# Performance work log

Hardware: AMD Instinct MI355X
Metric: run time of the kernel (lower is better)

Reference implementation:

```python
import jax, jax.numpy as jnp
import numpy as np
from jax.scipy.special import digamma, polygamma

N_ITERS = 100
TOL = 1e-3


def setup_inputs() -> dict:
    key = jax.random.key(0)
    x = jax.random.normal(key, (2_000_000, 10), dtype=jnp.float32)
    return {"x": x}


def reference(x):
    # x: [n, C] logits -> Dirichlet MLE over softmax probabilities
    p = jax.nn.softmax(x, axis=-1)            # [n, C]
    n = p.shape[0]
    m1 = p.mean(0)                            # [C] E[p]
    m2 = (p ** 2).mean(0)                     # [C] E[p^2]
    # method-of-moments initialization (as in the torch module)
    a0 = m1 * ((m1 - m2) / (m2 - m1 ** 2)).mean(-1)
    # loop-invariant sufficient statistic
    log_p_avg = jnp.log(p).mean(0)            # [C]

    def cond(carry):
        a, k, diff = carry
        return jnp.logical_and(k < N_ITERS, diff >= TOL)

    def body(carry):
        a, k, _ = carry
        g = (digamma(a.sum(-1)) - digamma(a) + log_p_avg) * n
        q = -n * polygamma(1, a)
        z = n * polygamma(1, a.sum(-1))
        q_inv = 1.0 / q
        b = (g * q_inv).sum(-1) / (1.0 / z + q_inv.sum(-1))
        a_new = a - (g - b) / q               # Newton step with rank-1 Hessian inverse
        diff = jnp.abs(a_new - a).sum()       # L1 norm, matches torch.norm(.,1)
        return (a_new, k + 1, diff)

    a, _, _ = jax.lax.while_loop(
        cond, body, (a0, jnp.int32(0), jnp.float32(jnp.inf))
    )
    return a.astype(jnp.float32)
```

## Files before the change

### kernel.cpp

```cpp
#include <hip/hip_runtime.h>
#include <math.h>

#define C 10
#define BLOCK 256
#define NBLOCKS 2048
#define TILE_ROWS 512
#define TILE_ELEMS (TILE_ROWS * C)
#define NSTATS (3 * C)


__device__ __forceinline__ void accum_row(const float* __restrict__ row,
                                          float* __restrict__ s1,
                                          float* __restrict__ s2,
                                          float* __restrict__ sl) {
  float v[C];
#pragma unroll
  for (int c = 0; c < C; c++) v[c] = row[c];
  float mx = v[0];
#pragma unroll
  for (int c = 1; c < C; c++) mx = fmaxf(mx, v[c]);
  float e[C], se = 0.f;
#pragma unroll
  for (int c = 0; c < C; c++) { v[c] -= mx; e[c] = __expf(v[c]); se += e[c]; }
  float inv = 1.0f / se;
  float lse = __logf(se);
#pragma unroll
  for (int c = 0; c < C; c++) {
    float p = e[c] * inv;
    s1[c] += p;
    s2[c] = fmaf(p, p, s2[c]);
    sl[c] += v[c] - lse;
  }
}

__global__ __launch_bounds__(BLOCK) void dir_stats_kernel(
    const float* __restrict__ x, float* __restrict__ partials,
    int nrows, int ntiles, int tailStart, int nblocks) {
  __shared__ float tile[TILE_ELEMS];
  const int tid = threadIdx.x;

  float s1[C], s2[C], sl[C];
#pragma unroll
  for (int c = 0; c < C; c++) { s1[c] = 0.f; s2[c] = 0.f; sl[c] = 0.f; }

  for (int t = blockIdx.x; t < ntiles; t += nblocks) {
    const float4* __restrict__ src = (const float4*)(x + (size_t)t * TILE_ELEMS);
    float4* dst = (float4*)tile;
#pragma unroll
    for (int i = 0; i < TILE_ELEMS / 4 / BLOCK; i++)
      dst[tid + i * BLOCK] = src[tid + i * BLOCK];
    __syncthreads();
#pragma unroll
    for (int r = 0; r < TILE_ROWS / BLOCK; r++)
      accum_row(tile + (size_t)(r * BLOCK + tid) * C, s1, s2, sl);
    __syncthreads();
  }

  if (blockIdx.x == nblocks - 1) {
    for (int rr = tailStart + tid; rr < nrows; rr += BLOCK)
      accum_row(x + (size_t)rr * C, s1, s2, sl);
  }

  const int lane = tid & 63;
  const int wave = tid >> 6;
  __shared__ float red[4][NSTATS];
#pragma unroll
  for (int c = 0; c < C; c++) {
    float v1 = s1[c], v2 = s2[c], v3 = sl[c];
#pragma unroll
    for (int off = 32; off >= 1; off >>= 1) {
      v1 += __shfl_down(v1, off);
      v2 += __shfl_down(v2, off);
      v3 += __shfl_down(v3, off);
    }
    if (lane == 0) {
      red[wave][c] = v1;
      red[wave][C + c] = v2;
      red[wave][2 * C + c] = v3;
    }
  }
  __syncthreads();
  if (tid < NSTATS) {
    float tot = red[0][tid] + red[1][tid] + red[2][tid] + red[3][tid];
    partials[(size_t)tid * nblocks + blockIdx.x] = tot;
  }
}


__device__ __forceinline__ void digtri8(double x, double& dg, double& tg) {
  double i0 = 1.0 / x,         i1 = 1.0 / (x + 1.0);
  double i2 = 1.0 / (x + 2.0), i3 = 1.0 / (x + 3.0);
  double i4 = 1.0 / (x + 4.0), i5 = 1.0 / (x + 5.0);
  double i6 = 1.0 / (x + 6.0), i7 = 1.0 / (x + 7.0);
  double rd = (i0 + i1) + (i2 + i3) + ((i4 + i5) + (i6 + i7));
  double rt = (i0 * i0 + i1 * i1) + (i2 * i2 + i3 * i3) +
              ((i4 * i4 + i5 * i5) + (i6 * i6 + i7 * i7));
  double y = x + 8.0;
  double yi = 1.0 / y, f = yi * yi;
  dg = log(y) - 0.5 * yi
     - f * (1.0 / 12 - f * (1.0 / 120 - f * (1.0 / 252 - f * (1.0 / 240 - f * (1.0 / 132)))))
     - rd;
  tg = rt + yi + 0.5 * f
     + f * yi * (1.0 / 6 - f * (1.0 / 30 - f * (1.0 / 42 - f * (1.0 / 30))));
}

__device__ __forceinline__ double wsum16(double v) {
#pragma unroll
  for (int off = 1; off < 16; off <<= 1) v += __shfl_xor(v, off);
  return v;
}

__global__ __launch_bounds__(1024) void dir_newton_kernel(
    const float* __restrict__ partials, float* __restrict__ out,
    int nparts, double nrows) {
  __shared__ double tot[NSTATS];
  const int tid = threadIdx.x;

  {
    const int j = tid >> 5;
    const int k = tid & 31;
    double s = 0.0;
    if (j < NSTATS) {
      const float* __restrict__ base = partials + (size_t)j * nparts;
#pragma unroll 8
      for (int b = k; b < nparts; b += 32)
        s += (double)base[b];
    }
#pragma unroll
    for (int off = 16; off >= 1; off >>= 1) s += __shfl_xor(s, off);
    if (j < NSTATS && k == 0) tot[j] = s;
  }
  __syncthreads();

  if (tid < 16) {
    const int c = tid;
    const bool act = (c < C);
    const double n = nrows;
    double m1 = 0.0, m2 = 0.0, lpa = 0.0;
    if (act) {
      m1 = tot[c] / n;
      m2 = tot[C + c] / n;
      lpa = tot[2 * C + c] / n;
    }
    double ratio = act ? (m1 - m2) / (m2 - m1 * m1) : 0.0;
    double rmean = wsum16(ratio) / (double)C;
    double a = act ? m1 * rmean : 0.0;

    double diff = 1e30;
    for (int k = 0; k < 100 && diff >= 1e-3; k++) {
      double S = wsum16(a);
      double dgl, tgl;
      digtri8(act ? a : S, dgl, tgl);
      double dgS = __shfl(dgl, 10);
      double tgS = __shfl(tgl, 10);
      double g = act ? (dgS - dgl + lpa) * n : 0.0;
      double qinv = act ? (-1.0) / (n * tgl) : 0.0;
      double z = n * tgS;
      double num = wsum16(g * qinv);
      double den = 1.0 / z + wsum16(qinv);
      double b = num / den;
      double anew = act ? a - (g - b) * qinv : 0.0;
      diff = wsum16(fabs(anew - a));
      a = anew;
    }
    if (act) out[c] = (float)a;
  }
}


extern "C" void kernel_launch(void* const* d_in, const int* in_sizes, int n_in,
                              void* d_out, int out_size, void* d_ws, size_t ws_size,
                              hipStream_t stream) {
  const float* x = (const float*)d_in[0];
  const int total = in_sizes[0];
  const int nrows = total / C;
  const int ntiles = nrows / TILE_ROWS;
  const int tailStart = ntiles * TILE_ROWS;

  int grid = NBLOCKS;
  size_t need = (size_t)NSTATS * grid * sizeof(float);
  if (need > ws_size) {
    grid = (int)(ws_size / (NSTATS * sizeof(float)));
    if (grid < 1) grid = 1;
  }

  float* partials = (float*)d_ws;
  dir_stats_kernel<<<grid, BLOCK, 0, stream>>>(x, partials, nrows, ntiles, tailStart, grid);
  dir_newton_kernel<<<1, 1024, 0, stream>>>(partials, (float*)d_out, grid, (double)nrows);
}
```

Baseline: 126.3 us.

## Double-buffer LDS tiles with register prefetch of the next tile

The stats kernel now keeps two LDS tile buffers and prefetches the next tile into registers while the current tile is processed. Raw s_barrier and waitcnt asm replace __syncthreads so the global loads can stay in flight across the barrier. The grid is halved to 1024 blocks, which gives each block more tiles to pipeline. This adds LDS use and register pressure, and the hand-written barriers carry a correctness risk.

```diff
diff --git a/kernel.cpp b/kernel.cpp
--- a/kernel.cpp
+++ b/kernel.cpp
@@ -3,7 +3,7 @@
 
 #define C 10
 #define BLOCK 256
-#define NBLOCKS 2048
+#define NBLOCKS 1024
 #define TILE_ROWS 512
 #define TILE_ELEMS (TILE_ROWS * C)
 #define NSTATS (3 * C)
@@ -33,27 +33,45 @@
   }
 }
 
+
 __global__ __launch_bounds__(BLOCK) void dir_stats_kernel(
     const float* __restrict__ x, float* __restrict__ partials,
     int nrows, int ntiles, int tailStart, int nblocks) {
-  __shared__ float tile[TILE_ELEMS];
+  __shared__ float buf[2][TILE_ELEMS];
+  __shared__ float red[4][NSTATS];
   const int tid = threadIdx.x;
 
   float s1[C], s2[C], sl[C];
 #pragma unroll
   for (int c = 0; c < C; c++) { s1[c] = 0.f; s2[c] = 0.f; sl[c] = 0.f; }
 
-  for (int t = blockIdx.x; t < ntiles; t += nblocks) {
+  float4 r0, r1, r2, r3, r4;
+  int t = blockIdx.x;
+  if (t < ntiles) {
     const float4* __restrict__ src = (const float4*)(x + (size_t)t * TILE_ELEMS);
-    float4* dst = (float4*)tile;
-#pragma unroll
-    for (int i = 0; i < TILE_ELEMS / 4 / BLOCK; i++)
-      dst[tid + i * BLOCK] = src[tid + i * BLOCK];
-    __syncthreads();
-#pragma unroll
-    for (int r = 0; r < TILE_ROWS / BLOCK; r++)
-      accum_row(tile + (size_t)(r * BLOCK + tid) * C, s1, s2, sl);
-    __syncthreads();
+    r0 = src[tid];        r1 = src[tid + 256];  r2 = src[tid + 512];
+    r3 = src[tid + 768];  r4 = src[tid + 1024];
+  }
+
+  int phase = 0;
+  for (; t < ntiles; t += nblocks, phase ^= 1) {
+    asm volatile("s_barrier" ::: "memory");
+
+    float4* dst = (float4*)buf[phase];
+    dst[tid]       = r0;  dst[tid + 256] = r1;  dst[tid + 512]  = r2;
+    dst[tid + 768] = r3;  dst[tid + 1024] = r4;
+
+    int tn = t + nblocks;
+    if (tn < ntiles) {
+      const float4* __restrict__ src = (const float4*)(x + (size_t)tn * TILE_ELEMS);
+      r0 = src[tid];        r1 = src[tid + 256];  r2 = src[tid + 512];
+      r3 = src[tid + 768];  r4 = src[tid + 1024];
+    }
+
+    asm volatile("s_waitcnt lgkmcnt(0)\n\ts_barrier" ::: "memory");
+
+    accum_row(buf[phase] + (size_t)tid * C, s1, s2, sl);
+    accum_row(buf[phase] + (size_t)(256 + tid) * C, s1, s2, sl);
   }
 
   if (blockIdx.x == nblocks - 1) {
@@ -63,7 +81,6 @@
 
   const int lane = tid & 63;
   const int wave = tid >> 6;
-  __shared__ float red[4][NSTATS];
 #pragma unroll
   for (int c = 0; c < C; c++) {
     float v1 = s1[c], v2 = s2[c], v3 = sl[c];
```

After: 122.7 us. 2.9% less time.

## Replace LDS tile staging with direct per-thread row-pair loads and register prefetch

Applied to the files above, without the earlier changes.

The stats kernel no longer stages tiles through shared memory behind block barriers. Each thread now loads two adjacent rows (20 floats) straight from global memory as five 16-byte nontemporal loads, and software-prefetches the next pair while it computes the current one. The grid is halved to 1024 blocks. The goal is to remove the LDS round trip and the barrier stalls and to overlap loads with compute, at the cost of more registers and strided per-thread access, which may reduce coalescing efficiency.

```diff
diff --git a/kernel.cpp b/kernel.cpp
--- a/kernel.cpp
+++ b/kernel.cpp
@@ -3,25 +3,22 @@
 
 #define C 10
 #define BLOCK 256
-#define NBLOCKS 2048
-#define TILE_ROWS 512
-#define TILE_ELEMS (TILE_ROWS * C)
+#define NBLOCKS 1024
 #define NSTATS (3 * C)
 
-
-__device__ __forceinline__ void accum_row(const float* __restrict__ row,
-                                          float* __restrict__ s1,
-                                          float* __restrict__ s2,
-                                          float* __restrict__ sl) {
-  float v[C];
-#pragma unroll
-  for (int c = 0; c < C; c++) v[c] = row[c];
+typedef float f4 __attribute__((ext_vector_type(4)));
+
+
+__device__ __forceinline__ void accum_vals(const float* __restrict__ v,
+                                           float* __restrict__ s1,
+                                           float* __restrict__ s2,
+                                           float* __restrict__ sl) {
   float mx = v[0];
 #pragma unroll
   for (int c = 1; c < C; c++) mx = fmaxf(mx, v[c]);
-  float e[C], se = 0.f;
-#pragma unroll
-  for (int c = 0; c < C; c++) { v[c] -= mx; e[c] = __expf(v[c]); se += e[c]; }
+  float w[C], e[C], se = 0.f;
+#pragma unroll
+  for (int c = 0; c < C; c++) { w[c] = v[c] - mx; e[c] = __expf(w[c]); se += e[c]; }
   float inv = 1.0f / se;
   float lse = __logf(se);
 #pragma unroll
@@ -29,36 +26,64 @@
     float p = e[c] * inv;
     s1[c] += p;
     s2[c] = fmaf(p, p, s2[c]);
-    sl[c] += v[c] - lse;
-  }
-}
+    sl[c] += w[c] - lse;
+  }
+}
+
 
 __global__ __launch_bounds__(BLOCK) void dir_stats_kernel(
     const float* __restrict__ x, float* __restrict__ partials,
-    int nrows, int ntiles, int tailStart, int nblocks) {
-  __shared__ float tile[TILE_ELEMS];
+    int nrows, int nblocks) {
   const int tid = threadIdx.x;
+  const int gid = blockIdx.x * BLOCK + tid;
+  const int stride = nblocks * BLOCK;
+  const int npairs = nrows >> 1;
 
   float s1[C], s2[C], sl[C];
 #pragma unroll
   for (int c = 0; c < C; c++) { s1[c] = 0.f; s2[c] = 0.f; sl[c] = 0.f; }
 
-  for (int t = blockIdx.x; t < ntiles; t += nblocks) {
-    const float4* __restrict__ src = (const float4*)(x + (size_t)t * TILE_ELEMS);
-    float4* dst = (float4*)tile;
-#pragma unroll
-    for (int i = 0; i < TILE_ELEMS / 4 / BLOCK; i++)
-      dst[tid + i * BLOCK] = src[tid + i * BLOCK];
-    __syncthreads();
-#pragma unroll
-    for (int r = 0; r < TILE_ROWS / BLOCK; r++)
-      accum_row(tile + (size_t)(r * BLOCK + tid) * C, s1, s2, sl);
-    __syncthreads();
-  }
-
-  if (blockIdx.x == nblocks - 1) {
-    for (int rr = tailStart + tid; rr < nrows; rr += BLOCK)
-      accum_row(x + (size_t)rr * C, s1, s2, sl);
+  int g = gid;
+  bool have = (g < npairs);
+  f4 a0 = 0, a1 = 0, a2 = 0, a3 = 0, a4 = 0;
+  if (have) {
+    const f4* __restrict__ p = (const f4*)(x + (size_t)g * 20);
+    a0 = __builtin_nontemporal_load(p);
+    a1 = __builtin_nontemporal_load(p + 1);
+    a2 = __builtin_nontemporal_load(p + 2);
+    a3 = __builtin_nontemporal_load(p + 3);
+    a4 = __builtin_nontemporal_load(p + 4);
+  }
+  while (have) {
+    const int gn = g + stride;
+    const bool haven = (gn < npairs);
+    f4 b0 = 0, b1 = 0, b2 = 0, b3 = 0, b4 = 0;
+    if (haven) {
+      const f4* __restrict__ p = (const f4*)(x + (size_t)gn * 20);
+      b0 = __builtin_nontemporal_load(p);
+      b1 = __builtin_nontemporal_load(p + 1);
+      b2 = __builtin_nontemporal_load(p + 2);
+      b3 = __builtin_nontemporal_load(p + 3);
+      b4 = __builtin_nontemporal_load(p + 4);
+    }
+    float v[20];
+    v[0]=a0.x; v[1]=a0.y; v[2]=a0.z; v[3]=a0.w;
+    v[4]=a1.x; v[5]=a1.y; v[6]=a1.z; v[7]=a1.w;
+    v[8]=a2.x; v[9]=a2.y; v[10]=a2.z; v[11]=a2.w;
+    v[12]=a3.x; v[13]=a3.y; v[14]=a3.z; v[15]=a3.w;
+    v[16]=a4.x; v[17]=a4.y; v[18]=a4.z; v[19]=a4.w;
+    accum_vals(v,      s1, s2, sl);
+    accum_vals(v + 10, s1, s2, sl);
+    a0 = b0; a1 = b1; a2 = b2; a3 = b3; a4 = b4;
+    g = gn; have = haven;
+  }
+
+  if ((nrows & 1) && gid == 0) {
+    float v[C];
+    const float* r = x + (size_t)(nrows - 1) * C;
+#pragma unroll
+    for (int c = 0; c < C; c++) v[c] = r[c];
+    accum_vals(v, s1, s2, sl);
   }
 
   const int lane = tid & 63;
@@ -174,8 +199,6 @@
   const float* x = (const float*)d_in[0];
   const int total = in_sizes[0];
   const int nrows = total / C;
-  const int ntiles = nrows / TILE_ROWS;
-  const int tailStart = ntiles * TILE_ROWS;
 
   int grid = NBLOCKS;
   size_t need = (size_t)NSTATS * grid * sizeof(float);
@@ -185,6 +208,6 @@
   }
 
   float* partials = (float*)d_ws;
-  dir_stats_kernel<<<grid, BLOCK, 0, stream>>>(x, partials, nrows, ntiles, tailStart, grid);
+  dir_stats_kernel<<<grid, BLOCK, 0, stream>>>(x, partials, nrows, grid);
   dir_newton_kernel<<<1, 1024, 0, stream>>>(partials, (float*)d_out, grid, (double)nrows);
 }
```

Result: slower. 137.0 us (+8.4%).

## Use per-wave LDS tiles with register prefetch instead of block-synchronized tiles

Applied to the files above, without the earlier changes.

Replaces the block-wide tile load with per-wave 128-row tiles staged through double-buffered LDS, prefetching the next tile into registers while computing the current one. This removes __syncthreads barriers and overlaps global loads with softmax math. The grid is halved to 1024 blocks. It relies on wave-level lockstep for LDS visibility across lanes.

```diff
diff --git a/kernel.cpp b/kernel.cpp
--- a/kernel.cpp
+++ b/kernel.cpp
@@ -3,10 +3,12 @@
 
 #define C 10
 #define BLOCK 256
-#define NBLOCKS 2048
-#define TILE_ROWS 512
-#define TILE_ELEMS (TILE_ROWS * C)
+#define NBLOCKS 1024
+#define WROWS 128
+#define WELEMS (WROWS * C)
 #define NSTATS (3 * C)
+
+typedef float f4 __attribute__((ext_vector_type(4)));
 
 
 __device__ __forceinline__ void accum_row(const float* __restrict__ row,
@@ -33,37 +35,69 @@
   }
 }
 
+
 __global__ __launch_bounds__(BLOCK) void dir_stats_kernel(
     const float* __restrict__ x, float* __restrict__ partials,
-    int nrows, int ntiles, int tailStart, int nblocks) {
-  __shared__ float tile[TILE_ELEMS];
+    int nrows, int nblocks) {
+  __shared__ float buf[4][2][WELEMS];
+  __shared__ float red[4][NSTATS];
   const int tid = threadIdx.x;
-
-  float s1[C], s2[C], sl[C];
-#pragma unroll
-  for (int c = 0; c < C; c++) { s1[c] = 0.f; s2[c] = 0.f; sl[c] = 0.f; }
-
-  for (int t = blockIdx.x; t < ntiles; t += nblocks) {
-    const float4* __restrict__ src = (const float4*)(x + (size_t)t * TILE_ELEMS);
-    float4* dst = (float4*)tile;
-#pragma unroll
-    for (int i = 0; i < TILE_ELEMS / 4 / BLOCK; i++)
-      dst[tid + i * BLOCK] = src[tid + i * BLOCK];
-    __syncthreads();
-#pragma unroll
-    for (int r = 0; r < TILE_ROWS / BLOCK; r++)
-      accum_row(tile + (size_t)(r * BLOCK + tid) * C, s1, s2, sl);
-    __syncthreads();
-  }
-
-  if (blockIdx.x == nblocks - 1) {
-    for (int rr = tailStart + tid; rr < nrows; rr += BLOCK)
-      accum_row(x + (size_t)rr * C, s1, s2, sl);
-  }
-
   const int lane = tid & 63;
   const int wave = tid >> 6;
-  __shared__ float red[4][NSTATS];
+
+  const int gwave = blockIdx.x * 4 + wave;
+  const int wstride = nblocks * 4;
+  const int ntiles = nrows / WROWS;
+  const int tailStart = ntiles * WROWS;
+
+  float s1[C], s2[C], sl[C];
+#pragma unroll
+  for (int c = 0; c < C; c++) { s1[c] = 0.f; s2[c] = 0.f; sl[c] = 0.f; }
+
+  int g = gwave;
+  f4 a0 = 0, a1 = 0, a2 = 0, a3 = 0, a4 = 0;
+  if (g < ntiles) {
+    const f4* __restrict__ p = (const f4*)(x + (size_t)g * WELEMS) + lane;
+    a0 = p[0]; a1 = p[64]; a2 = p[128]; a3 = p[192]; a4 = p[256];
+  }
+  int phase = 0;
+  while (g < ntiles) {
+    f4* dst = (f4*)buf[wave][phase] + lane;
+    dst[0] = a0; dst[64] = a1; dst[128] = a2; dst[192] = a3; dst[256] = a4;
+
+    const int gn = g + wstride;
+    if (gn < ntiles) {
+      const f4* __restrict__ p = (const f4*)(x + (size_t)gn * WELEMS) + lane;
+      a0 = p[0]; a1 = p[64]; a2 = p[128]; a3 = p[192]; a4 = p[256];
+    }
+
+    accum_row(buf[wave][phase] + (size_t)lane * C, s1, s2, sl);
+    accum_row(buf[wave][phase] + (size_t)(64 + lane) * C, s1, s2, sl);
+
+    g = gn; phase ^= 1;
+  }
+
+  if (gwave == wstride - 1) {
+    for (int rr = tailStart + lane; rr < nrows; rr += 64) {
+      float v[C];
+      const float* r = x + (size_t)rr * C;
+#pragma unroll
+      for (int c = 0; c < C; c++) v[c] = r[c];
+      float mx = v[0];
+#pragma unroll
+      for (int c = 1; c < C; c++) mx = fmaxf(mx, v[c]);
+      float e[C], se = 0.f;
+#pragma unroll
+      for (int c = 0; c < C; c++) { v[c] -= mx; e[c] = __expf(v[c]); se += e[c]; }
+      float inv = 1.0f / se, lse = __logf(se);
+#pragma unroll
+      for (int c = 0; c < C; c++) {
+        float p = e[c] * inv;
+        s1[c] += p; s2[c] = fmaf(p, p, s2[c]); sl[c] += v[c] - lse;
+      }
+    }
+  }
+
 #pragma unroll
   for (int c = 0; c < C; c++) {
     float v1 = s1[c], v2 = s2[c], v3 = sl[c];
@@ -174,8 +208,6 @@
   const float* x = (const float*)d_in[0];
   const int total = in_sizes[0];
   const int nrows = total / C;
-  const int ntiles = nrows / TILE_ROWS;
-  const int tailStart = ntiles * TILE_ROWS;
 
   int grid = NBLOCKS;
   size_t need = (size_t)NSTATS * grid * sizeof(float);
@@ -185,6 +217,6 @@
   }
 
   float* partials = (float*)d_ws;
-  dir_stats_kernel<<<grid, BLOCK, 0, stream>>>(x, partials, nrows, ntiles, tailStart, grid);
+  dir_stats_kernel<<<grid, BLOCK, 0, stream>>>(x, partials, nrows, grid);
   dir_newton_kernel<<<1, 1024, 0, stream>>>(partials, (float*)d_out, grid, (double)nrows);
 }
```

Result: faster. 122.0 us (-3.5%).
